# Performance work log

Hardware: AMD Instinct MI355X
Metric: run time of the kernel (lower is better)

The kernel has to match this reference:

```python
import jax, jax.numpy as jnp
import numpy as np

B, F, D, U = 4096, 32, 64, 256


def setup_inputs() -> dict:
    key = jax.random.key(0)
    k1, k2, k3, k4 = jax.random.split(key, 4)
    embeds = jax.random.normal(k1, (B, F, D), dtype=jnp.float32)
    # glorot-ish scaling for the learned weights
    linear_w = jax.random.normal(k2, (F * D, U), dtype=jnp.float32) * (2.0 / (F * D + U)) ** 0.5
    inner_w = jax.random.normal(k3, (U, F), dtype=jnp.float32) * (2.0 / (U + F)) ** 0.5
    outer_w = jax.random.normal(k4, (U, D, D), dtype=jnp.float32) * (2.0 / (2 * D)) ** 0.5
    return {"embeds": embeds, "linear_w": linear_w, "inner_w": inner_w, "outer_w": outer_w}


def reference(embeds, linear_w, inner_w, outer_w):
    b = embeds.shape[0]
    # linear signal lz: flatten fields and project -> [B, U]
    lz = embeds.reshape(b, -1) @ linear_w
    # inner products: per unit u, delta_u = sum_f w_{u,f} * e_f  -> [B, U, D];
    # lp_inner[b,u] = ||delta_u||^2 (collapses the per-unit TF loop into one einsum)
    delta = jnp.einsum('bfd,uf->bud', embeds, inner_w)
    lp_inner = jnp.sum(jnp.square(delta), axis=2)  # [B, U]
    # outer products: product = fs fs^T with fs = sum_f e_f; lp_outer[b,u] = <product_b, W_u>
    fs = jnp.sum(embeds, axis=1)  # [B, D]
    lp_outer = jnp.einsum('bi,bj,uij->bu', fs, fs, outer_w)  # [B, U]
    return jnp.concatenate([lz, lp_inner, lp_outer], axis=1)  # [B, 3U]
```

## Files before the change

kernel.cpp:

```cpp
#include <hip/hip_runtime.h>
#include <hip/hip_bf16.h>


#define KA 3072
#define KW 7168

typedef __attribute__((ext_vector_type(8))) short short8v;
typedef __attribute__((ext_vector_type(4))) float f32x4;

#define GLOAD(src, dst) __builtin_amdgcn_global_load_lds( \
    (const __attribute__((address_space(1))) void*)(src), \
    (__attribute__((address_space(3))) void*)(dst), 16, 0, 0)

static __device__ __forceinline__ short f2bf(float f) {
    union { float f; unsigned u; } v; v.f = f;
    unsigned r = v.u + 0x7fffu + ((v.u >> 16) & 1u);
    return (short)(r >> 16);
}
static __device__ __forceinline__ float bf2f(short s) {
    union { unsigned u; float f; } v; v.u = ((unsigned)(unsigned short)s) << 16;
    return v.f;
}
static __device__ __forceinline__ int cvtpk(float lo, float hi) {
    int r;
    asm("v_cvt_pk_bf16_f32 %0, %1, %2" : "=v"(r) : "v"(lo), "v"(hi));
    return r;
}

__global__ __launch_bounds__(256) void prep(const float* __restrict__ embeds,
                                            const float* __restrict__ lw,
                                            const float* __restrict__ iw,
                                            const float* __restrict__ ow,
                                            short* __restrict__ A,
                                            short* __restrict__ FST,
                                            short* __restrict__ Wt,
                                            float4* __restrict__ outv) {
    __shared__ float se[2048];
    __shared__ short sebf[2048];
    int t = threadIdx.x;

    if (blockIdx.x >= 4352) {
        int idx = (blockIdx.x - 4352) * 256 + t;
        int row = idx >> 6, c4 = idx & 63;
        outv[(size_t)row * 192 + 128 + c4] = (float4){0.f, 0.f, 0.f, 0.f};
        return;
    }

    if (blockIdx.x < 4096) {
        int b = blockIdx.x;
        const float* e = embeds + (size_t)b * 2048;
        short* arow = A + (size_t)b * KA;

        float4 v0 = ((const float4*)e)[t * 2];
        float4 v1 = ((const float4*)e)[t * 2 + 1];
        ((float4*)se)[t * 2] = v0;
        ((float4*)se)[t * 2 + 1] = v1;
        short8v sb;
        sb[0] = f2bf(v0.x); sb[1] = f2bf(v0.y); sb[2] = f2bf(v0.z); sb[3] = f2bf(v0.w);
        sb[4] = f2bf(v1.x); sb[5] = f2bf(v1.y); sb[6] = f2bf(v1.z); sb[7] = f2bf(v1.w);
        ((short8v*)sebf)[t] = sb;
        *(short8v*)&arow[t * 8] = sb;

        __syncthreads();
        if (t < 64) {
            float s = 0.f;
            #pragma unroll
            for (int f = 0; f < 32; ++f) s += se[f * 64 + t];
            FST[((size_t)(b >> 7)) * 8192 + t * 128 + (b & 127)] = f2bf(s);
        }

        int wid = t >> 6, lane = t & 63;
        int tm = wid >> 1, tn = wid & 1;
        int lr = lane & 15, lk = (lane >> 4) * 8;
        f32x4 g = {0.f, 0.f, 0.f, 0.f};
        #pragma unroll
        for (int ks = 0; ks < 2; ++ks) {
            short8v a  = *(const short8v*)&sebf[(tm * 16 + lr) * 64 + ks * 32 + lk];
            short8v bb = *(const short8v*)&sebf[(tn * 16 + lr) * 64 + ks * 32 + lk];
            g = __builtin_amdgcn_mfma_f32_16x16x32_bf16(a, bb, g, 0, 0, 0);
        }
        #pragma unroll
        for (int r = 0; r < 4; ++r) {
            int grow = tm * 16 + (lane >> 4) * 4 + r;
            int gcol = tn * 16 + lr;
            arow[2048 + grow * 32 + gcol] = f2bf(g[r]);
        }
    } else {
        int u = blockIdx.x - 4096;
        short* w = Wt + (size_t)u * KW;

        for (int k = t; k < 2048; k += 256) w[k] = f2bf(lw[(size_t)k * 256 + u]);

        if (t < 32) se[t] = iw[u * 32 + t];
        __syncthreads();
        for (int idx = t; idx < 1024; idx += 256)
            w[2048 + idx] = f2bf(se[idx >> 5] * se[idx & 31]);

        const float* owu = ow + (size_t)u * 4096;
        for (int i = t; i < 512; i += 256) {
            float4 a = ((const float4*)owu)[i * 2];
            float4 b = ((const float4*)owu)[i * 2 + 1];
            short8v s;
            s[0] = f2bf(a.x); s[1] = f2bf(a.y); s[2] = f2bf(a.z); s[3] = f2bf(a.w);
            s[4] = f2bf(b.x); s[5] = f2bf(b.y); s[6] = f2bf(b.z); s[7] = f2bf(b.w);
            *(short8v*)&w[3072 + i * 8] = s;
        }
    }
}

__global__ __launch_bounds__(256) void gemm_tile(const short* __restrict__ A,
                                                 const short* __restrict__ Wt,
                                                 const short* __restrict__ FST,
                                                 float* __restrict__ out) {
    __shared__ short As[2][8192];
    __shared__ short Bs[2][4096];

    int id = blockIdx.x;
    int xcd = id & 7, s = id >> 3;
    int seg, mtl, nt, kc, nk;
    if (s < 16)      { seg = 0; mtl = s & 3;  nt = s >> 2;        kc = 0;       nk = 32; }
    else if (s < 32) { int q = s - 16; seg = 1; mtl = q & 3; nt = q >> 2;       kc = 0;  nk = 16; }
    else             { int q = s - 32; seg = 2; mtl = q & 3; nt = (q >> 2) & 3; kc = q >> 4; nk = 16; }
    int mt = xcd * 4 + mtl;
    int brow = mt * 128, bcol = nt * 64;
    int akoff = (seg == 0) ? 0 : 2048;
    int boff  = (seg == 0) ? 0 : (seg == 1) ? 2048 : 3072 + kc * 1024;

    int t = threadIdx.x, w = t >> 6, lane = t & 63;
    int lr = lane & 15, hi = lane >> 4;
    int srow = t >> 3;
    int soct = (t & 7) ^ (srow & 7);

    const short* Asrc = A  + (size_t)(brow + srow) * KA + akoff + soct * 8;
    const short* Bsrc = Wt + (size_t)(bcol + srow) * KW + boff  + soct * 8;
    const short* Fsrc = FST + (size_t)mt * 8192;

    auto stageA = [&](int p, int kt) {
        #pragma unroll
        for (int i = 0; i < 4; ++i)
            GLOAD(Asrc + (size_t)i * 32 * KA + kt * 64, &As[p][i * 2048 + t * 8]);
    };
    auto stageB = [&](int p, int kt) {
        #pragma unroll
        for (int i = 0; i < 2; ++i)
            GLOAD(Bsrc + (size_t)i * 32 * KW + kt * 64, &Bs[p][i * 2048 + t * 8]);
    };

    f32x4 acc[2][4];
    #pragma unroll
    for (int m = 0; m < 2; ++m)
        #pragma unroll
        for (int n = 0; n < 4; ++n) acc[m][n] = (f32x4){0.f, 0.f, 0.f, 0.f};

    auto compute = [&](const short* a_s, const short* b_s) {
        #pragma unroll
        for (int ks = 0; ks < 2; ++ks) {
            int oct = ((ks * 4 + hi) ^ (lr & 7)) * 8;
            short8v a[2], b[4];
            #pragma unroll
            for (int m = 0; m < 2; ++m)
                a[m] = *(const short8v*)&a_s[(w * 32 + m * 16 + lr) * 64 + oct];
            #pragma unroll
            for (int n = 0; n < 4; ++n)
                b[n] = *(const short8v*)&b_s[(n * 16 + lr) * 64 + oct];
            __builtin_amdgcn_s_setprio(1);
            #pragma unroll
            for (int m = 0; m < 2; ++m)
                #pragma unroll
                for (int n = 0; n < 4; ++n)
                    acc[m][n] = __builtin_amdgcn_mfma_f32_16x16x32_bf16(a[m], b[n], acc[m][n], 0, 0, 0);
            __builtin_amdgcn_s_setprio(0);
        }
    };

    if (seg != 2) {
        stageA(0, 0); stageB(0, 0);
        stageA(1, 1); stageB(1, 1);
        __builtin_amdgcn_sched_barrier(0);
        for (int kt = 0; kt < nk; ++kt) {
            int cur = kt & 1;
            if (kt + 1 < nk) asm volatile("s_waitcnt vmcnt(6)" ::: "memory");
            else             asm volatile("s_waitcnt vmcnt(0)" ::: "memory");
            __builtin_amdgcn_s_barrier();
            __builtin_amdgcn_sched_barrier(0);
            compute(As[cur], Bs[cur]);
            __builtin_amdgcn_sched_barrier(0);
            __builtin_amdgcn_s_barrier();
            if (kt + 2 < nk) { stageA(cur, kt + 2); stageB(cur, kt + 2); }
            __builtin_amdgcn_sched_barrier(0);
        }
    } else {
        #pragma unroll
        for (int i = 0; i < 4; ++i)
            GLOAD(Fsrc + i * 2048 + t * 8, &As[0][i * 2048 + t * 8]);
        stageB(0, 0); stageB(1, 1);
        asm volatile("s_waitcnt vmcnt(4)" ::: "memory");
        __builtin_amdgcn_s_barrier();
        __builtin_amdgcn_sched_barrier(0);

        float fj[2][2][8];
        #pragma unroll
        for (int m = 0; m < 2; ++m) {
            int row = w * 32 + m * 16 + lr;
            #pragma unroll
            for (int ks = 0; ks < 2; ++ks) {
                int j0 = (ks * 4 + hi) * 8;
                #pragma unroll
                for (int e = 0; e < 8; ++e)
                    fj[m][ks][e] = bf2f(As[0][(j0 + e) * 128 + row]);
            }
        }
        for (int kt = 0; kt < nk; ++kt) {
            int cur = kt & 1;
            if (kt + 1 < nk) asm volatile("s_waitcnt vmcnt(2)" ::: "memory");
            else             asm volatile("s_waitcnt vmcnt(0)" ::: "memory");
            __builtin_amdgcn_s_barrier();
            __builtin_amdgcn_sched_barrier(0);
            int iidx = kc * 16 + kt;
            float sv[2];
            #pragma unroll
            for (int m = 0; m < 2; ++m)
                sv[m] = bf2f(As[0][iidx * 128 + w * 32 + m * 16 + lr]);
            #pragma unroll
            for (int ks = 0; ks < 2; ++ks) {
                int oct = ((ks * 4 + hi) ^ (lr & 7)) * 8;
                short8v b[4];
                #pragma unroll
                for (int n = 0; n < 4; ++n)
                    b[n] = *(const short8v*)&Bs[cur][(n * 16 + lr) * 64 + oct];
                #pragma unroll
                for (int m = 0; m < 2; ++m) {
                    union { int i32[4]; short8v v; } fa;
                    #pragma unroll
                    for (int q2 = 0; q2 < 4; ++q2)
                        fa.i32[q2] = cvtpk(sv[m] * fj[m][ks][2 * q2], sv[m] * fj[m][ks][2 * q2 + 1]);
                    __builtin_amdgcn_s_setprio(1);
                    #pragma unroll
                    for (int n = 0; n < 4; ++n)
                        acc[m][n] = __builtin_amdgcn_mfma_f32_16x16x32_bf16(fa.v, b[n], acc[m][n], 0, 0, 0);
                    __builtin_amdgcn_s_setprio(0);
                }
            }
            __builtin_amdgcn_sched_barrier(0);
            __builtin_amdgcn_s_barrier();
            if (kt + 2 < nk) stageB(cur, kt + 2);
            __builtin_amdgcn_sched_barrier(0);
        }
    }

    int segbase = seg * 256;
    if (seg != 2) {
        #pragma unroll
        for (int m = 0; m < 2; ++m) {
            int row0 = brow + w * 32 + m * 16 + hi * 4;
            #pragma unroll
            for (int n = 0; n < 4; ++n) {
                int col = segbase + bcol + n * 16 + lr;
                #pragma unroll
                for (int r = 0; r < 4; ++r)
                    out[(size_t)(row0 + r) * 768 + col] = acc[m][n][r];
            }
        }
    } else {
        #pragma unroll
        for (int m = 0; m < 2; ++m) {
            int row0 = brow + w * 32 + m * 16 + hi * 4;
            #pragma unroll
            for (int n = 0; n < 4; ++n) {
                int col = segbase + bcol + n * 16 + lr;
                #pragma unroll
                for (int r = 0; r < 4; ++r)
                    unsafeAtomicAdd(&out[(size_t)(row0 + r) * 768 + col], acc[m][n][r]);
            }
        }
    }
}

extern "C" void kernel_launch(void* const* d_in, const int* in_sizes, int n_in,
                              void* d_out, int out_size, void* d_ws, size_t ws_size,
                              hipStream_t stream) {
    const float* embeds = (const float*)d_in[0];
    const float* lw = (const float*)d_in[1];
    const float* iw = (const float*)d_in[2];
    const float* ow = (const float*)d_in[3];
    float* out = (float*)d_out;

    short* A   = (short*)d_ws;
    short* Wt  = A + (size_t)4096 * KA;
    short* FST = Wt + (size_t)256 * KW;

    prep<<<dim3(5376), dim3(256), 0, stream>>>(embeds, lw, iw, ow, A, FST, Wt, (float4*)out);
    gemm_tile<<<dim3(768), dim3(256), 0, stream>>>(A, Wt, FST, out);
}
```

Measured before the change: 56.33 us.

## Process four batch rows per prep block with one wave per row

The prep kernel now gives each wavefront one batch row, so a block handles four rows instead of one and the grid drops from 5376 to 2304 blocks. Field sums move from a serial LDS loop to register accumulation plus cross-lane shuffles, and the Gram MFMA tiles are computed per wave from wave-private LDS, which removes the block-wide barrier. This cuts block launch overhead and synchronisation but gives each wave more serial MFMA work and longer per-thread load chains.

```diff
diff --git a/kernel.cpp b/kernel.cpp
--- a/kernel.cpp
+++ b/kernel.cpp
@@ -35,66 +35,88 @@
                                             short* __restrict__ FST,
                                             short* __restrict__ Wt,
                                             float4* __restrict__ outv) {
-    __shared__ float se[2048];
-    __shared__ short sebf[2048];
+    __shared__ short sebf[4][2048];
+    __shared__ float sew[32];
     int t = threadIdx.x;
 
-    if (blockIdx.x >= 4352) {
-        int idx = (blockIdx.x - 4352) * 256 + t;
+    if (blockIdx.x >= 1280) {
+        int idx = (blockIdx.x - 1280) * 256 + t;
         int row = idx >> 6, c4 = idx & 63;
         outv[(size_t)row * 192 + 128 + c4] = (float4){0.f, 0.f, 0.f, 0.f};
         return;
     }
 
-    if (blockIdx.x < 4096) {
-        int b = blockIdx.x;
+    if (blockIdx.x < 1024) {
+        int row = t >> 6, lane = t & 63;
+        int b = blockIdx.x * 4 + row;
         const float* e = embeds + (size_t)b * 2048;
         short* arow = A + (size_t)b * KA;
 
-        float4 v0 = ((const float4*)e)[t * 2];
-        float4 v1 = ((const float4*)e)[t * 2 + 1];
-        ((float4*)se)[t * 2] = v0;
-        ((float4*)se)[t * 2 + 1] = v1;
-        short8v sb;
-        sb[0] = f2bf(v0.x); sb[1] = f2bf(v0.y); sb[2] = f2bf(v0.z); sb[3] = f2bf(v0.w);
-        sb[4] = f2bf(v1.x); sb[5] = f2bf(v1.y); sb[6] = f2bf(v1.z); sb[7] = f2bf(v1.w);
-        ((short8v*)sebf)[t] = sb;
-        *(short8v*)&arow[t * 8] = sb;
-
-        __syncthreads();
-        if (t < 64) {
-            float s = 0.f;
-            #pragma unroll
-            for (int f = 0; f < 32; ++f) s += se[f * 64 + t];
-            FST[((size_t)(b >> 7)) * 8192 + t * 128 + (b & 127)] = f2bf(s);
-        }
-
-        int wid = t >> 6, lane = t & 63;
-        int tm = wid >> 1, tn = wid & 1;
+        float4 fa[4], fb[4];
+        #pragma unroll
+        for (int j = 0; j < 4; ++j) {
+            fa[j] = ((const float4*)e)[2 * lane + j * 128];
+            fb[j] = ((const float4*)e)[2 * lane + 1 + j * 128];
+        }
+        #pragma unroll
+        for (int j = 0; j < 4; ++j) {
+            short8v sb;
+            sb[0] = f2bf(fa[j].x); sb[1] = f2bf(fa[j].y);
+            sb[2] = f2bf(fa[j].z); sb[3] = f2bf(fa[j].w);
+            sb[4] = f2bf(fb[j].x); sb[5] = f2bf(fb[j].y);
+            sb[6] = f2bf(fb[j].z); sb[7] = f2bf(fb[j].w);
+            *(short8v*)&arow[8 * lane + j * 512] = sb;
+            *(short8v*)&sebf[row][8 * lane + j * 512] = sb;
+        }
+        float ps[8];
+        #pragma unroll
+        for (int j = 0; j < 4; ++j) {
+            float v[8] = {fa[j].x, fa[j].y, fa[j].z, fa[j].w,
+                          fb[j].x, fb[j].y, fb[j].z, fb[j].w};
+            #pragma unroll
+            for (int e2 = 0; e2 < 8; ++e2) ps[e2] = (j == 0) ? v[e2] : ps[e2] + v[e2];
+        }
+        #pragma unroll
+        for (int m = 8; m <= 32; m <<= 1)
+            #pragma unroll
+            for (int e2 = 0; e2 < 8; ++e2) ps[e2] += __shfl_xor(ps[e2], m, 64);
+        if (lane < 8) {
+            #pragma unroll
+            for (int e2 = 0; e2 < 8; ++e2) {
+                int d = 8 * lane + e2;
+                FST[((size_t)(b >> 7)) * 8192 + d * 128 + (b & 127)] = f2bf(ps[e2]);
+            }
+        }
+
         int lr = lane & 15, lk = (lane >> 4) * 8;
-        f32x4 g = {0.f, 0.f, 0.f, 0.f};
-        #pragma unroll
-        for (int ks = 0; ks < 2; ++ks) {
-            short8v a  = *(const short8v*)&sebf[(tm * 16 + lr) * 64 + ks * 32 + lk];
-            short8v bb = *(const short8v*)&sebf[(tn * 16 + lr) * 64 + ks * 32 + lk];
-            g = __builtin_amdgcn_mfma_f32_16x16x32_bf16(a, bb, g, 0, 0, 0);
-        }
-        #pragma unroll
-        for (int r = 0; r < 4; ++r) {
-            int grow = tm * 16 + (lane >> 4) * 4 + r;
-            int gcol = tn * 16 + lr;
-            arow[2048 + grow * 32 + gcol] = f2bf(g[r]);
-        }
+        #pragma unroll
+        for (int tm = 0; tm < 2; ++tm)
+            #pragma unroll
+            for (int tn = 0; tn < 2; ++tn) {
+                f32x4 g = {0.f, 0.f, 0.f, 0.f};
+                #pragma unroll
+                for (int ks = 0; ks < 2; ++ks) {
+                    short8v a  = *(const short8v*)&sebf[row][(tm * 16 + lr) * 64 + ks * 32 + lk];
+                    short8v bb = *(const short8v*)&sebf[row][(tn * 16 + lr) * 64 + ks * 32 + lk];
+                    g = __builtin_amdgcn_mfma_f32_16x16x32_bf16(a, bb, g, 0, 0, 0);
+                }
+                #pragma unroll
+                for (int r = 0; r < 4; ++r) {
+                    int grow = tm * 16 + (lane >> 4) * 4 + r;
+                    int gcol = tn * 16 + lr;
+                    arow[2048 + grow * 32 + gcol] = f2bf(g[r]);
+                }
+            }
     } else {
-        int u = blockIdx.x - 4096;
+        int u = blockIdx.x - 1024;
         short* w = Wt + (size_t)u * KW;
 
         for (int k = t; k < 2048; k += 256) w[k] = f2bf(lw[(size_t)k * 256 + u]);
 
-        if (t < 32) se[t] = iw[u * 32 + t];
+        if (t < 32) sew[t] = iw[u * 32 + t];
         __syncthreads();
         for (int idx = t; idx < 1024; idx += 256)
-            w[2048 + idx] = f2bf(se[idx >> 5] * se[idx & 31]);
+            w[2048 + idx] = f2bf(sew[idx >> 5] * sew[idx & 31]);
 
         const float* owu = ow + (size_t)u * 4096;
         for (int i = t; i < 512; i += 256) {
@@ -289,6 +311,6 @@
     short* Wt  = A + (size_t)4096 * KA;
     short* FST = Wt + (size_t)256 * KW;
 
-    prep<<<dim3(5376), dim3(256), 0, stream>>>(embeds, lw, iw, ow, A, FST, Wt, (float4*)out);
+    prep<<<dim3(2304), dim3(256), 0, stream>>>(embeds, lw, iw, ow, A, FST, Wt, (float4*)out);
     gemm_tile<<<dim3(768), dim3(256), 0, stream>>>(A, Wt, FST, out);
 }
```

Result: no change. 55.52 us, median of 2 (-1.4%).
